# Kernel tuning notes

Hardware: AMD Instinct MI355X
Metric: run time of the kernel (lower is better)

Reference implementation:

```python
import jax, jax.numpy as jnp
import numpy as np


def _rbf_forward(batches, centers, beta, W, b):
    # Pairwise Euclidean distances via GEMM expansion instead of materializing
    # the O(n*K*dim) difference tensor the torch code builds.
    x2 = jnp.sum(batches * batches, axis=1, keepdims=True)          # [n, 1]
    c2 = jnp.sum(centers * centers, axis=1)                          # [K]
    xc = jnp.einsum('nd,kd->nk', batches, centers)                   # [n, K]
    d2 = jnp.maximum(x2 + c2[None, :] - 2.0 * xc, 0.0)               # [n, K]
    dist = jnp.sqrt(d2)
    radial = jnp.exp(-beta * dist)                                   # beta: [1, K]
    return radial @ W.T + b                                          # [n, num_class]


def setup_inputs() -> dict:
    key = jax.random.key(0)
    k1, k2, k3, k4, k5 = jax.random.split(key, 5)
    n, K, dim, num_class = 16384, 2048, 512, 10
    batches = jax.random.normal(k1, (n, dim), dtype=jnp.float32)
    centers = jax.random.normal(k2, (K, dim), dtype=jnp.float32)
    beta = jnp.full((1, K), 0.1, dtype=jnp.float32)  # torch init: ones/10
    W = jax.random.normal(k4, (num_class, K), dtype=jnp.float32) / np.sqrt(K)
    b = jax.random.normal(k5, (num_class,), dtype=jnp.float32) * 0.01
    return {"batches": batches, "centers": centers, "beta": beta, "W": W, "b": b}


def reference(batches, centers, beta, W, b):
    return _rbf_forward(batches, centers, beta, W, b)
```

## Files before the change

kernel.cpp:

```cpp
#include <hip/hip_runtime.h>
#include <hip/hip_bf16.h>
#include <stdint.h>

#define M_N  16384
#define K_C  2048
#define DIM  512
#define NCLS 10
#define NBN  (K_C / 128)

typedef unsigned short u16;
typedef float  f32x4  __attribute__((ext_vector_type(4)));
typedef __bf16 bf16x8 __attribute__((ext_vector_type(8)));


__device__ __forceinline__ void async_ld16(const void* g, void* l) {
  __builtin_amdgcn_global_load_lds(
      (const __attribute__((address_space(1))) void*)g,
      (__attribute__((address_space(3))) void*)l,
      16, 0, 0);
}

__device__ __forceinline__ u16 f2bf_rne(float f) {
  uint32_t u = __float_as_uint(f);
  u += 0x7FFFu + ((u >> 16) & 1u);
  return (u16)(u >> 16);
}


#define NPREP ((M_N + K_C) / 2)

__global__ __launch_bounds__(256) void prep(
    const float4* __restrict__ batches, const float4* __restrict__ centers,
    const float* __restrict__ W,
    ushort4* __restrict__ Abf, ushort4* __restrict__ Bbf,
    float* __restrict__ x2, float* __restrict__ c2, u16* __restrict__ Wbf) {
  int b = blockIdx.x, t = threadIdx.x;
  if (b < NPREP) {
    int rp = b * 2 + (t >> 7);
    int col = t & 127;
    const float4* src; ushort4* dst; float* sq; int row;
    if (rp < M_N) { src = batches; dst = Abf; sq = x2; row = rp; }
    else          { src = centers; dst = Bbf; sq = c2; row = rp - M_N; }
    float4 v = src[(size_t)row * 128 + col];
    float ss = v.x * v.x + v.y * v.y + v.z * v.z + v.w * v.w;
    ushort4 o;
    o.x = f2bf_rne(v.x); o.y = f2bf_rne(v.y);
    o.z = f2bf_rne(v.z); o.w = f2bf_rne(v.w);
    dst[(size_t)row * 128 + col] = o;
    ss += __shfl_down(ss, 32);
    ss += __shfl_down(ss, 16);
    ss += __shfl_down(ss, 8);
    ss += __shfl_down(ss, 4);
    ss += __shfl_down(ss, 2);
    ss += __shfl_down(ss, 1);
    __shared__ float part[4];
    if ((t & 63) == 0) part[t >> 6] = ss;
    __syncthreads();
    if (t == 0) sq[row] = part[0] + part[1];
    if (t == 128) sq[row] = part[2] + part[3];
  } else {
    int wb = b - NPREP;
#pragma unroll
    for (int i = 0; i < 4; ++i) {
      int idx = wb * 1024 + i * 256 + t;
      int n = idx >> 11, k = idx & 2047;
      Wbf[idx] = (n < NCLS) ? f2bf_rne(W[n * K_C + k]) : (u16)0;
    }
  }
}


__global__ __launch_bounds__(256, 4) void rbf_main(
    const u16* __restrict__ A,
    const u16* __restrict__ B,
    const float* __restrict__ x2,
    const float* __restrict__ c2,
    const float* __restrict__ beta,
    const u16* __restrict__ Wbf,
    float* __restrict__ partial) {
  constexpr int BK = 64;
  __shared__ alignas(16) unsigned char smem[32768];
  u16* As = (u16*)smem;
  u16* Bs = (u16*)(smem + 16384);
  u16* Rt = (u16*)smem;

  const int tid  = threadIdx.x;
  const int lane = tid & 63;
  const int wid  = tid >> 6;
  const int bid = blockIdx.x;
  const int g = bid >> 3, r8 = bid & 7;
  const int bm = r8 * 16 + (g & 15);
  const int bn = g >> 4;
  const int row0 = bm * 128, col0 = bn * 128;
  const int wrC = (wid >> 1) * 64;
  const int wcB = (wid & 1) * 64;

  f32x4 acc[4][4] = {};

  const int srow = tid >> 3;
  const int scol = ((tid & 7) ^ (srow & 7)) * 8;
  const u16* aG = A + (size_t)(row0 + srow) * DIM + scol;
  const u16* bG = B + (size_t)(col0 + srow) * DIM + scol;
  u16* aL = As + tid * 8;
  u16* bL = Bs + tid * 8;

  const int frow = lane & 15;
  const int fq   = lane >> 4;
  const int fsw  = frow & 7;

  for (int k0 = 0; k0 < DIM; k0 += BK) {
    __syncthreads();
#pragma unroll
    for (int i = 0; i < 4; ++i) {
      async_ld16(aG + k0 + i * 32 * DIM, aL + i * 2048);
      async_ld16(bG + k0 + i * 32 * DIM, bL + i * 2048);
    }
    __syncthreads();

#pragma unroll
    for (int kh = 0; kh < 2; ++kh) {
      const int slot = ((kh << 2) | fq) ^ fsw;
      bf16x8 cf[4], bfr[4];
#pragma unroll
      for (int mi = 0; mi < 4; ++mi)
        cf[mi] = *(const bf16x8*)(Bs + (wrC + mi * 16 + frow) * BK + slot * 8);
#pragma unroll
      for (int ni = 0; ni < 4; ++ni)
        bfr[ni] = *(const bf16x8*)(As + (wcB + ni * 16 + frow) * BK + slot * 8);
#pragma unroll
      for (int mi = 0; mi < 4; ++mi)
#pragma unroll
        for (int ni = 0; ni < 4; ++ni)
          acc[mi][ni] = __builtin_amdgcn_mfma_f32_16x16x32_bf16(
              cf[mi], bfr[ni], acc[mi][ni], 0, 0, 0);
    }
  }

  const int cls = lane & 15, q = lane >> 4;
  float4 c2q[4], btq[4];
#pragma unroll
  for (int mi = 0; mi < 4; ++mi) {
    int base = col0 + wrC + mi * 16 + q * 4;
    c2q[mi] = *(const float4*)(c2 + base);
    btq[mi] = *(const float4*)(beta + base);
  }
  float x2v[4];
#pragma unroll
  for (int ni = 0; ni < 4; ++ni)
    x2v[ni] = x2[row0 + wcB + ni * 16 + cls];

  __syncthreads();

  union Pack { u16 h[4]; uint2 v; };
#pragma unroll
  for (int mi = 0; mi < 4; ++mi) {
#pragma unroll
    for (int ni = 0; ni < 4; ++ni) {
      Pack pk;
#pragma unroll
      for (int r = 0; r < 4; ++r) {
        float xc = acc[mi][ni][r];
        float d2 = fmaxf(x2v[ni] + c2q[mi][r] - 2.0f * xc, 0.0f);
        float radial = __expf(-btq[mi][r] * sqrtf(d2));
        pk.h[r] = f2bf_rne(radial);
      }
      int br  = wcB + ni * 16 + cls;
      int cc0 = wrC + mi * 16 + q * 4;
      *(uint2*)(Rt + br * 128 + (cc0 ^ ((br & 15) << 3))) = pk.v;
    }
  }
  __syncthreads();

  bf16x8 wfr[4];
#pragma unroll
  for (int t = 0; t < 4; ++t)
    wfr[t] = *(const bf16x8*)(Wbf + (size_t)cls * K_C + col0 + t * 32 + q * 8);

  f32x4 acc2[2] = {};
#pragma unroll
  for (int s2 = 0; s2 < 2; ++s2) {
    const int br = (wid * 2 + s2) * 16 + cls;
    const u16* rrow = Rt + br * 128;
    const int sw = cls << 3;
#pragma unroll
    for (int t = 0; t < 4; ++t) {
      bf16x8 ra = *(const bf16x8*)(rrow + ((t * 32 + q * 8) ^ sw));
      acc2[s2] = __builtin_amdgcn_mfma_f32_16x16x32_bf16(
          ra, wfr[t], acc2[s2], 0, 0, 0);
    }
  }

#pragma unroll
  for (int s2 = 0; s2 < 2; ++s2)
#pragma unroll
    for (int r = 0; r < 4; ++r) {
      int gr = row0 + (wid * 2 + s2) * 16 + q * 4 + r;
      partial[(size_t)gr * (NBN * 16) + bn * 16 + cls] = acc2[s2][r];
    }
}


__global__ __launch_bounds__(256) void reduce_out(
    const float* __restrict__ partial, const float* __restrict__ b,
    float* __restrict__ out) {
  int lane = threadIdx.x & 63;
  int row = blockIdx.x * 4 + (threadIdx.x >> 6);
  float4 v = ((const float4*)(partial + (size_t)row * (NBN * 16)))[lane];
#pragma unroll
  for (int m = 4; m < 64; m <<= 1) {
    v.x += __shfl_xor(v.x, m);
    v.y += __shfl_xor(v.y, m);
    v.z += __shfl_xor(v.z, m);
    v.w += __shfl_xor(v.w, m);
  }
  int c = lane & 3;
  if (lane < 2) {
    float4 bq = ((const float4*)b)[c];
    v.x += bq.x; v.y += bq.y; v.z += bq.z; v.w += bq.w;
    ((float2*)(out + (size_t)row * NCLS + c * 4))[0] = {v.x, v.y};
    ((float2*)(out + (size_t)row * NCLS + c * 4 + 2))[0] = {v.z, v.w};
  } else if (lane == 2) {
    float2 o = {v.x + b[8], v.y + b[9]};
    *(float2*)(out + (size_t)row * NCLS + 8) = o;
  }
}


extern "C" void kernel_launch(void* const* d_in, const int* in_sizes, int n_in,
                              void* d_out, int out_size, void* d_ws, size_t ws_size,
                              hipStream_t stream) {
  const float* batches = (const float*)d_in[0];
  const float* centers = (const float*)d_in[1];
  const float* beta    = (const float*)d_in[2];
  const float* W       = (const float*)d_in[3];
  const float* bias    = (const float*)d_in[4];
  float* out = (float*)d_out;

  char* ws = (char*)d_ws;
  u16*  Abf = (u16*)ws;
  u16*  Bbf = (u16*)(ws + (size_t)M_N * DIM * 2);
  float* x2 = (float*)(ws + (size_t)(M_N + K_C) * DIM * 2);
  float* c2 = x2 + M_N;
  u16*  Wbf = (u16*)(c2 + K_C);
  float* partial = (float*)((char*)Wbf + 16 * K_C * 2);

  prep<<<dim3(NPREP + 32), dim3(256), 0, stream>>>(
      (const float4*)batches, (const float4*)centers, W,
      (ushort4*)Abf, (ushort4*)Bbf, x2, c2, Wbf);
  rbf_main<<<dim3(NBN * (M_N / 128)), dim3(256), 0, stream>>>(
      Abf, Bbf, x2, c2, beta, Wbf, partial);
  reduce_out<<<dim3(M_N / 4), dim3(256), 0, stream>>>(partial, bias, out);
}
```

Measured before the change: 148.5 us.

## Fuse final reduction into main kernel via last-block atomic counter

Removes the separate reduce_out launch. Each main block writes its partial logits, then bumps a per-row-tile atomic counter. The last of the 16 column blocks for that row tile sums all partials, adds the bias and writes the output. This saves one kernel launch and its gap, at the cost of a threadfence, an atomic, and a serial 32-row reduction loop in the final block of each row tile. The partial buffer layout is changed to bn-major so that reduction can use it.

```diff
diff --git a/kernel.cpp b/kernel.cpp
--- a/kernel.cpp
+++ b/kernel.cpp
@@ -6,7 +6,8 @@
 #define K_C  2048
 #define DIM  512
 #define NCLS 10
-#define NBN  (K_C / 128)
+#define NBN  16
+#define NBM  (M_N / 128)
 
 typedef unsigned short u16;
 typedef float  f32x4  __attribute__((ext_vector_type(4)));
@@ -33,7 +34,8 @@
     const float4* __restrict__ batches, const float4* __restrict__ centers,
     const float* __restrict__ W,
     ushort4* __restrict__ Abf, ushort4* __restrict__ Bbf,
-    float* __restrict__ x2, float* __restrict__ c2, u16* __restrict__ Wbf) {
+    float* __restrict__ x2, float* __restrict__ c2, u16* __restrict__ Wbf,
+    int* __restrict__ cnt) {
   int b = blockIdx.x, t = threadIdx.x;
   if (b < NPREP) {
     int rp = b * 2 + (t >> 7);
@@ -66,6 +68,7 @@
       int n = idx >> 11, k = idx & 2047;
       Wbf[idx] = (n < NCLS) ? f2bf_rne(W[n * K_C + k]) : (u16)0;
     }
+    if (wb == 0 && t < NBM) cnt[t] = 0;
   }
 }
 
@@ -77,9 +80,13 @@
     const float* __restrict__ c2,
     const float* __restrict__ beta,
     const u16* __restrict__ Wbf,
-    float* __restrict__ partial) {
+    const float* __restrict__ bias,
+    float* __restrict__ partial,
+    int* __restrict__ cnt,
+    float* __restrict__ out) {
   constexpr int BK = 64;
   __shared__ alignas(16) unsigned char smem[32768];
+  __shared__ int lastFlag;
   u16* As = (u16*)smem;
   u16* Bs = (u16*)(smem + 16384);
   u16* Rt = (u16*)smem;
@@ -195,33 +202,42 @@
 #pragma unroll
     for (int r = 0; r < 4; ++r) {
       int gr = row0 + (wid * 2 + s2) * 16 + q * 4 + r;
-      partial[(size_t)gr * (NBN * 16) + bn * 16 + cls] = acc2[s2][r];
-    }
-}
-
-
-__global__ __launch_bounds__(256) void reduce_out(
-    const float* __restrict__ partial, const float* __restrict__ b,
-    float* __restrict__ out) {
-  int lane = threadIdx.x & 63;
-  int row = blockIdx.x * 4 + (threadIdx.x >> 6);
-  float4 v = ((const float4*)(partial + (size_t)row * (NBN * 16)))[lane];
-#pragma unroll
-  for (int m = 4; m < 64; m <<= 1) {
-    v.x += __shfl_xor(v.x, m);
-    v.y += __shfl_xor(v.y, m);
-    v.z += __shfl_xor(v.z, m);
-    v.w += __shfl_xor(v.w, m);
-  }
-  int c = lane & 3;
-  if (lane < 2) {
-    float4 bq = ((const float4*)b)[c];
-    v.x += bq.x; v.y += bq.y; v.z += bq.z; v.w += bq.w;
-    ((float2*)(out + (size_t)row * NCLS + c * 4))[0] = {v.x, v.y};
-    ((float2*)(out + (size_t)row * NCLS + c * 4 + 2))[0] = {v.z, v.w};
-  } else if (lane == 2) {
-    float2 o = {v.x + b[8], v.y + b[9]};
-    *(float2*)(out + (size_t)row * NCLS + 8) = o;
+      partial[((size_t)bn * M_N + gr) * 16 + cls] = acc2[s2][r];
+    }
+
+  __syncthreads();
+  __threadfence();
+  if (tid == 0) {
+    int prev = atomicAdd(&cnt[bm], 1);
+    lastFlag = (prev == NBN - 1);
+  }
+  __syncthreads();
+  if (!lastFlag) return;
+  __threadfence();
+
+  const int bnl = lane >> 2, quad = lane & 3;
+  float4 bq = {0.f, 0.f, 0.f, 0.f};
+  if (quad == 0)      bq = *(const float4*)(bias);
+  else if (quad == 1) bq = *(const float4*)(bias + 4);
+  else if (quad == 2) { bq.x = bias[8]; bq.y = bias[9]; }
+  for (int rr = 0; rr < 32; ++rr) {
+    int row = row0 + wid * 32 + rr;
+    const float* p = partial + ((size_t)bnl * M_N + row) * 16 + quad * 4;
+    float4 v = *(const float4*)p;
+#pragma unroll
+    for (int m = 4; m < 64; m <<= 1) {
+      v.x += __shfl_xor(v.x, m);
+      v.y += __shfl_xor(v.y, m);
+      v.z += __shfl_xor(v.z, m);
+      v.w += __shfl_xor(v.w, m);
+    }
+    if (lane < 2) {
+      float* o = out + (size_t)row * NCLS + quad * 4;
+      *(float2*)o       = {v.x + bq.x, v.y + bq.y};
+      *(float2*)(o + 2) = {v.z + bq.z, v.w + bq.w};
+    } else if (lane == 2) {
+      *(float2*)(out + (size_t)row * NCLS + 8) = {v.x + bq.x, v.y + bq.y};
+    }
   }
 }
 
@@ -242,12 +258,12 @@
   float* x2 = (float*)(ws + (size_t)(M_N + K_C) * DIM * 2);
   float* c2 = x2 + M_N;
   u16*  Wbf = (u16*)(c2 + K_C);
-  float* partial = (float*)((char*)Wbf + 16 * K_C * 2);
+  int*  cnt = (int*)((char*)Wbf + 16 * K_C * 2);
+  float* partial = (float*)((char*)cnt + 1024);
 
   prep<<<dim3(NPREP + 32), dim3(256), 0, stream>>>(
       (const float4*)batches, (const float4*)centers, W,
-      (ushort4*)Abf, (ushort4*)Bbf, x2, c2, Wbf);
-  rbf_main<<<dim3(NBN * (M_N / 128)), dim3(256), 0, stream>>>(
-      Abf, Bbf, x2, c2, beta, Wbf, partial);
-  reduce_out<<<dim3(M_N / 4), dim3(256), 0, stream>>>(partial, bias, out);
-}
+      (ushort4*)Abf, (ushort4*)Bbf, x2, c2, Wbf, cnt);
+  rbf_main<<<dim3(NBN * NBM), dim3(256), 0, stream>>>(
+      Abf, Bbf, x2, c2, beta, Wbf, bias, partial, cnt, out);
+}
```

New measurement: 392.8 us. 165% more time.
